# Kernel optimization log

Measured on AMD Instinct MI355X. Metric: run time of the kernel, lower is better.

The kernel has to match this reference:

```python
import jax, jax.numpy as jnp
import numpy as np

H = 16        # heads
DH = 64       # dim_head
DM = 1024     # query_dim = context_dim
INNER = H * DH


def setup_inputs() -> dict:
    key = jax.random.key(0)
    ks = jax.random.split(key, 5)
    s = 0.02
    queries = jax.random.normal(ks[0], (2, 2048, DM), dtype=jnp.float32)
    Wq = jax.random.normal(ks[1], (DM, INNER), dtype=jnp.float32) * s
    Wkv = jax.random.normal(ks[2], (DM, 2 * INNER), dtype=jnp.float32) * s
    Wo = jax.random.normal(ks[3], (INNER, DM), dtype=jnp.float32) * s
    bo = jax.random.normal(ks[4], (DM,), dtype=jnp.float32) * s
    return {"queries": queries, "Wq": Wq, "Wkv": Wkv, "Wo": Wo, "bo": bo}


def reference(queries, Wq, Wkv, Wo, bo):
    b, n, _ = queries.shape
    scale = DH ** -0.5
    q = queries @ Wq                       # [b, n, inner]
    kv = queries @ Wkv                     # self-attention: context = queries
    k, v = jnp.split(kv, 2, axis=-1)
    # b n (h d) -> b h n d
    split_heads = lambda t: t.reshape(b, n, H, DH).transpose(0, 2, 1, 3)
    q, k, v = map(split_heads, (q, k, v))
    sim = jnp.einsum('bhid,bhjd->bhij', q, k) * scale
    attn = jax.nn.softmax(sim, axis=-1)    # dropout is identity (p=0 / eval)
    out = jnp.einsum('bhij,bhjd->bhid', attn, v)
    out = out.transpose(0, 2, 1, 3).reshape(b, n, INNER)
    return out @ Wo + bo
```

## Files before the change

kernel.cpp:

```cpp
#include <hip/hip_runtime.h>
#include <math.h>
#include <stdint.h>

typedef _Float16 half8v __attribute__((ext_vector_type(8)));
typedef _Float16 half4v __attribute__((ext_vector_type(4)));
typedef _Float16 half2v __attribute__((ext_vector_type(2)));
typedef __fp16 fp16x2 __attribute__((ext_vector_type(2)));
typedef float floatx4 __attribute__((ext_vector_type(4)));

#define MFMA16(a, b, c) __builtin_amdgcn_mfma_f32_16x16x32_f16(a, b, c, 0, 0, 0)

#define QSCALE 0.18033688011112f

__device__ __forceinline__ void gld_lds16(const void* g, void* l) {
  __builtin_amdgcn_global_load_lds(
      (const __attribute__((address_space(1))) uint32_t*)(uintptr_t)g,
      (__attribute__((address_space(3))) uint32_t*)(uintptr_t)l, 16, 0, 0);
}

__device__ __forceinline__ half2v pk16(float a, float b) {
  fp16x2 t = __builtin_amdgcn_cvt_pkrtz(a, b);
  return __builtin_bit_cast(half2v, t);
}

__device__ __forceinline__ int swz(int row, int blk) {
  return row * 64 + ((blk ^ (row & 7)) << 3);
}

__device__ __forceinline__ int vswz(int row, int blk) {
  return row * 32 + ((blk ^ ((row >> 1) & 3)) << 3);
}

__device__ __forceinline__ int gswz(int row, int blk) {
  return row * 32 + ((blk ^ ((row >> 1) & 3)) << 3);
}

__global__ __launch_bounds__(256) void prep(
    const float* __restrict__ X, const float* __restrict__ Wq,
    const float* __restrict__ Wkv, const float* __restrict__ Wo,
    _Float16* __restrict__ X16, _Float16* __restrict__ WqkvT,
    _Float16* __restrict__ WoT)
{
  __shared__ alignas(16) _Float16 Tt[64 * 68];
  const int bid = blockIdx.x;
  if (bid < 2048) {
    size_t gid = (size_t)bid * 256 + threadIdx.x;
    const float4* src = (const float4*)(X) + gid * 2;
    float4 a = src[0], b = src[1];
    half8v h;
    h[0]=(_Float16)a.x; h[1]=(_Float16)a.y; h[2]=(_Float16)a.z; h[3]=(_Float16)a.w;
    h[4]=(_Float16)b.x; h[5]=(_Float16)b.y; h[6]=(_Float16)b.z; h[7]=(_Float16)b.w;
    *((half8v*)X16 + gid) = h;
    return;
  }
  int b = bid - 2048;
  const float* src; _Float16* dst; int N, tk, tn;
  if (b < 256)      { src = Wq;  dst = WqkvT;                 N = 1024; tk = b & 15;        tn = b >> 4; }
  else if (b < 768) { src = Wkv; dst = WqkvT + (size_t)1024 * 1024; N = 2048; tk = (b - 256) & 15; tn = (b - 256) >> 4; }
  else              { src = Wo;  dst = WoT;                   N = 1024; tk = (b - 768) & 15; tn = (b - 768) >> 4; }

  const int t = threadIdx.x;
  {
    int kg = t >> 4, ng = t & 15;
    const float* sp = src + (size_t)(tk * 64 + kg * 4) * N + tn * 64 + ng * 4;
    float4 r0 = *(const float4*)(sp);
    float4 r1 = *(const float4*)(sp + N);
    float4 r2 = *(const float4*)(sp + 2 * N);
    float4 r3 = *(const float4*)(sp + 3 * N);
    half4v h;
    h[0]=(_Float16)r0.x; h[1]=(_Float16)r1.x; h[2]=(_Float16)r2.x; h[3]=(_Float16)r3.x;
    *(half4v*)&Tt[(ng * 4 + 0) * 68 + kg * 4] = h;
    h[0]=(_Float16)r0.y; h[1]=(_Float16)r1.y; h[2]=(_Float16)r2.y; h[3]=(_Float16)r3.y;
    *(half4v*)&Tt[(ng * 4 + 1) * 68 + kg * 4] = h;
    h[0]=(_Float16)r0.z; h[1]=(_Float16)r1.z; h[2]=(_Float16)r2.z; h[3]=(_Float16)r3.z;
    *(half4v*)&Tt[(ng * 4 + 2) * 68 + kg * 4] = h;
    h[0]=(_Float16)r0.w; h[1]=(_Float16)r1.w; h[2]=(_Float16)r2.w; h[3]=(_Float16)r3.w;
    *(half4v*)&Tt[(ng * 4 + 3) * 68 + kg * 4] = h;
  }
  __syncthreads();
  #pragma unroll
  for (int i = 0; i < 2; i++) {
    int idx = t + i * 256;
    int nl = idx >> 3, k8 = (idx & 7) * 8;
    half8v v = *(half8v*)&Tt[nl * 68 + k8];
    *(half8v*)(dst + (size_t)(tn * 64 + nl) * 1024 + tk * 64 + k8) = v;
  }
}

__global__ __launch_bounds__(256) void qkv_gemm(
    const _Float16* __restrict__ X16, const _Float16* __restrict__ WqkvT,
    _Float16* __restrict__ q_ws, _Float16* __restrict__ k_ws,
    _Float16* __restrict__ vT_ws)
{
  constexpr int K = 1024;
  __shared__ alignas(16) _Float16 Tt[128 * 136];
  _Float16* As = Tt;
  _Float16* Bs = Tt + 4096;

  const int m0 = blockIdx.x * 128;
  const int n0 = blockIdx.y * 128;

  const int tid  = threadIdx.x;
  const int wave = tid >> 6, lane = tid & 63;
  const int qd = lane >> 4, l15 = lane & 15;
  const int wr = (wave >> 1) * 64, wc = (wave & 1) * 64;
  const int r0i = tid >> 2;
  const int cbs = (((tid & 3) ^ ((r0i >> 1) & 3))) * 8;

  floatx4 acc[4][4] = {};

  for (int k0 = 0; k0 < K; k0 += 32) {
    gld_lds16(X16 + (size_t)(m0 + r0i) * K + k0 + cbs, &As[tid * 8]);
    gld_lds16(X16 + (size_t)(m0 + 64 + r0i) * K + k0 + cbs, &As[(tid + 256) * 8]);
    gld_lds16(WqkvT + (size_t)(n0 + r0i) * K + k0 + cbs, &Bs[tid * 8]);
    gld_lds16(WqkvT + (size_t)(n0 + 64 + r0i) * K + k0 + cbs, &Bs[(tid + 256) * 8]);
    __syncthreads();
    half8v a[4], b[4];
    #pragma unroll
    for (int it = 0; it < 4; it++)
      a[it] = *(half8v*)&As[gswz(wr + it * 16 + l15, qd)];
    #pragma unroll
    for (int jt = 0; jt < 4; jt++)
      b[jt] = *(half8v*)&Bs[gswz(wc + jt * 16 + l15, qd)];
    #pragma unroll
    for (int it = 0; it < 4; it++)
      #pragma unroll
      for (int jt = 0; jt < 4; jt++)
        acc[it][jt] = MFMA16(a[it], b[jt], acc[it][jt]);
    __syncthreads();
  }

  if (n0 < 2048) {
    #pragma unroll
    for (int it = 0; it < 4; it++) {
      #pragma unroll
      for (int jt = 0; jt < 4; jt++) {
        #pragma unroll
        for (int r = 0; r < 4; r++) {
          int m = m0 + wr + it * 16 + qd * 4 + r;
          int n = n0 + wc + jt * 16 + l15;
          float val = acc[it][jt][r];
          int bb = m >> 11, nn = m & 2047;
          if (n0 < 1024) {
            int h = n >> 6, d = n & 63;
            q_ws[(((size_t)bb * 16 + h) * 2048 + nn) * 64 + d] = (_Float16)(val * QSCALE);
          } else {
            int c = n - 1024, h = c >> 6, d = c & 63;
            k_ws[(((size_t)bb * 16 + h) * 2048 + nn) * 64 + d] = (_Float16)val;
          }
        }
      }
    }
  } else {
    #pragma unroll
    for (int it = 0; it < 4; it++) {
      #pragma unroll
      for (int jt = 0; jt < 4; jt++) {
        #pragma unroll
        for (int r = 0; r < 4; r++) {
          int ml = wr + it * 16 + qd * 4 + r;
          int nl = wc + jt * 16 + l15;
          Tt[nl * 136 + ml] = (_Float16)acc[it][jt][r];
        }
      }
    }
    __syncthreads();
    int row = tid >> 1;
    int mh  = (tid & 1) * 64;
    int c   = (n0 - 2048) + row;
    int bb  = m0 >> 11;
    int nnb = (m0 & 2047) + mh;
    _Float16* dstp =
        vT_ws + (((size_t)bb * 16 + (c >> 6)) * 64 + (c & 63)) * 2048 + nnb;
    #pragma unroll
    for (int i = 0; i < 8; i++)
      *(half8v*)(dstp + i * 8) = *(half8v*)&Tt[row * 136 + mh + i * 8];
  }
}

__global__ __launch_bounds__(256, 2) void attn_kernel(
    const _Float16* __restrict__ q_ws, const _Float16* __restrict__ k_ws,
    const _Float16* __restrict__ vT_ws, _Float16* __restrict__ aout)
{
  constexpr int N = 2048;
  __shared__ alignas(16) char smem[66560];
  _Float16* Kbase = (_Float16*)smem;
  _Float16* Vbase = (_Float16*)(smem + 32768);
  _Float16* PQ    = (_Float16*)(smem + 49152);

  const int id = blockIdx.x;
  const int bh = ((id >> 8) << 3) | (id & 7);
  const int qt = (id >> 3) & 31;

  const _Float16* Qp = q_ws + (size_t)bh * N * 64;
  const _Float16* Kp = k_ws + (size_t)bh * N * 64;
  const _Float16* Vp = vT_ws + (size_t)bh * 64 * N;

  const int tid = threadIdx.x, wave = tid >> 6, lane = tid & 63;
  const int qd = lane >> 4, l15 = lane & 15;
  const int q0 = qt * 64;
  const int wkv = wave * 32;

  _Float16* Ps = PQ + wave * 2048;
  _Float16* Vs = Vbase + wave * 2048;

  const int krr = lane >> 3, kcb = (lane & 7) ^ krr;
  const int vrr = lane >> 2, vcb = (lane & 3) ^ ((lane >> 3) & 3);

  auto stage_k = [&](int il, int buf) {
    const _Float16* src = Kp + (size_t)(wkv + il * 128) * 64;
    _Float16* dst = Kbase + (wave * 2 + buf) * 2048;
    #pragma unroll
    for (int j = 0; j < 4; j++)
      gld_lds16(src + (size_t)(j * 8 + krr) * 64 + kcb * 8,
                dst + (j * 64 + lane) * 8);
  };
  auto stage_v = [&](int il) {
    const _Float16* src = Vp + wkv + il * 128;
    #pragma unroll
    for (int j = 0; j < 4; j++)
      gld_lds16(src + (size_t)(j * 16 + (vrr & 15)) * N + vcb * 8,
                Vs + (j * 64 + lane) * 8);
  };

  #pragma unroll
  for (int i = 0; i < 2; i++) {
    int idx = tid + i * 256;
    int r = idx >> 3, cb = (idx ^ r) & 7;
    gld_lds16(Qp + (size_t)(q0 + r) * 64 + cb * 8, PQ + idx * 8);
  }
  stage_k(0, 0);
  stage_v(0);
  stage_k(1, 1);

  asm volatile("s_waitcnt vmcnt(12)" ::: "memory");
  __builtin_amdgcn_s_barrier();
  __builtin_amdgcn_sched_barrier(0);

  half8v qf[4][2];
  #pragma unroll
  for (int m = 0; m < 4; m++)
    #pragma unroll
    for (int ks = 0; ks < 2; ks++)
      qf[m][ks] = *(half8v*)&PQ[swz(m * 16 + l15, ks * 4 + qd)];

  asm volatile("s_waitcnt lgkmcnt(0)" ::: "memory");
  __builtin_amdgcn_s_barrier();
  __builtin_amdgcn_sched_barrier(0);

  const half8v ones = {(_Float16)1, (_Float16)1, (_Float16)1, (_Float16)1,
                       (_Float16)1, (_Float16)1, (_Float16)1, (_Float16)1};
  floatx4 o[4][4] = {};
  floatx4 ol[4] = {};

  #pragma unroll 2
  for (int i = 0; i < 16; ++i) {
    if (i < 15) asm volatile("s_waitcnt vmcnt(8)" ::: "memory");
    else        asm volatile("s_waitcnt vmcnt(4)" ::: "memory");
    __builtin_amdgcn_sched_barrier(0);

    const _Float16* Kb = Kbase + (wave * 2 + (i & 1)) * 2048;

    floatx4 s[2][4] = {};
    #pragma unroll
    for (int ks = 0; ks < 2; ks++) {
      half8v kf0 = *(half8v*)&Kb[swz(l15, ks * 4 + qd)];
      half8v kf1 = *(half8v*)&Kb[swz(16 + l15, ks * 4 + qd)];
      __builtin_amdgcn_s_setprio(1);
      #pragma unroll
      for (int m = 0; m < 4; m++) {
        s[0][m] = MFMA16(kf0, qf[m][ks], s[0][m]);
        s[1][m] = MFMA16(kf1, qf[m][ks], s[1][m]);
      }
      __builtin_amdgcn_s_setprio(0);
    }

    #pragma unroll
    for (int m = 0; m < 4; m++)
      #pragma unroll
      for (int nt = 0; nt < 2; nt++) {
        float p0 = __builtin_amdgcn_exp2f(s[nt][m][0]);
        float p1 = __builtin_amdgcn_exp2f(s[nt][m][1]);
        float p2 = __builtin_amdgcn_exp2f(s[nt][m][2]);
        float p3 = __builtin_amdgcn_exp2f(s[nt][m][3]);
        half2v h01 = pk16(p0, p1);
        half2v h23 = pk16(p2, p3);
        half4v pk;
        pk[0] = h01[0]; pk[1] = h01[1]; pk[2] = h23[0]; pk[3] = h23[1];
        *(half4v*)&Ps[vswz(m * 16 + l15, 2 * nt + (qd >> 1)) + (qd & 1) * 4] = pk;
      }

    if (i < 15) asm volatile("s_waitcnt vmcnt(4)" ::: "memory");
    else        asm volatile("s_waitcnt vmcnt(0)" ::: "memory");
    __builtin_amdgcn_sched_barrier(0);

    half8v pf[4], vfr[4];
    #pragma unroll
    for (int m = 0; m < 4; m++)
      pf[m] = *(half8v*)&Ps[vswz(m * 16 + l15, qd)];
    #pragma unroll
    for (int dt = 0; dt < 4; dt++)
      vfr[dt] = *(half8v*)&Vs[vswz(dt * 16 + l15, qd)];

    asm volatile("s_waitcnt lgkmcnt(0)" ::: "memory");
    __builtin_amdgcn_sched_barrier(0);

    if (i <= 14) stage_v(i + 1);
    if (i <= 13) stage_k(i + 2, i & 1);
    __builtin_amdgcn_sched_barrier(0);

    __builtin_amdgcn_s_setprio(1);
    #pragma unroll
    for (int m = 0; m < 4; m++)
      ol[m] = MFMA16(pf[m], ones, ol[m]);
    #pragma unroll
    for (int m = 0; m < 4; m++)
      #pragma unroll
      for (int dt = 0; dt < 4; dt++)
        o[m][dt] = MFMA16(pf[m], vfr[dt], o[m][dt]);
    __builtin_amdgcn_s_setprio(0);
  }

  __syncthreads();
  float* sc    = (float*)smem;
  float* ls_sc = (float*)(smem + 65536);
  float* myp = sc + wave * 4096;
  #pragma unroll
  for (int m = 0; m < 4; m++)
    #pragma unroll
    for (int r = 0; r < 4; r++) {
      int row = m * 16 + qd * 4 + r;
      myp[row * 64 +  0 + l15] = o[m][0][r];
      myp[row * 64 + 16 + l15] = o[m][1][r];
      myp[row * 64 + 32 + l15] = o[m][2][r];
      myp[row * 64 + 48 + l15] = o[m][3][r];
      ls_sc[wave * 64 + row] = ol[m][r];
    }
  __syncthreads();

  const int bb = bh >> 4, hh = bh & 15;
  #pragma unroll
  for (int j = 0; j < 4; j++) {
    int row = wave * 16 + j * 4 + qd;
    floatx4 a0 = *(floatx4*)&sc[(size_t)(0 * 64 + row) * 64 + l15 * 4];
    floatx4 a1 = *(floatx4*)&sc[(size_t)(1 * 64 + row) * 64 + l15 * 4];
    floatx4 a2 = *(floatx4*)&sc[(size_t)(2 * 64 + row) * 64 + l15 * 4];
    floatx4 a3 = *(floatx4*)&sc[(size_t)(3 * 64 + row) * 64 + l15 * 4];
    floatx4 sum = (a0 + a1) + (a2 + a3);
    float ls = ls_sc[row] + ls_sc[64 + row] + ls_sc[128 + row] + ls_sc[192 + row];
    float inv = 1.0f / ls;
    half2v h01 = pk16(sum[0] * inv, sum[1] * inv);
    half2v h23 = pk16(sum[2] * inv, sum[3] * inv);
    half4v hv;
    hv[0] = h01[0]; hv[1] = h01[1]; hv[2] = h23[0]; hv[3] = h23[1];
    *(half4v*)(aout + ((size_t)(bb * 2048 + q0 + row)) * 1024 + hh * 64 + l15 * 4) = hv;
  }
}

__global__ __launch_bounds__(256) void out_gemm(
    const _Float16* __restrict__ A, const _Float16* __restrict__ WoT,
    const float* __restrict__ bo, float* __restrict__ Out)
{
  constexpr int K = 1024;
  __shared__ alignas(16) _Float16 As[64 * 64];
  __shared__ alignas(16) _Float16 Bs[128 * 64];

  const int m0 = blockIdx.x * 64;
  const int n0 = blockIdx.y * 128;
  const int tid = threadIdx.x;
  const int wave = tid >> 6, lane = tid & 63;
  const int qd = lane >> 4, l15 = lane & 15;
  const int wr = (wave >> 1) * 32, wc = (wave & 1) * 64;

  floatx4 acc[2][4] = {};

  for (int k0 = 0; k0 < K; k0 += 64) {
    #pragma unroll
    for (int i = 0; i < 2; i++) {
      int idx = tid + i * 256;
      int r = idx >> 3, cb = (idx ^ r) & 7;
      gld_lds16(A + (size_t)(m0 + r) * K + k0 + cb * 8, &As[idx * 8]);
    }
    #pragma unroll
    for (int i = 0; i < 4; i++) {
      int idx = tid + i * 256;
      int r = idx >> 3, cb = (idx ^ r) & 7;
      gld_lds16(WoT + (size_t)(n0 + r) * K + k0 + cb * 8, &Bs[idx * 8]);
    }
    __syncthreads();
    half8v a[2][2], b[4][2];
    #pragma unroll
    for (int it = 0; it < 2; it++)
      #pragma unroll
      for (int ks = 0; ks < 2; ks++)
        a[it][ks] = *(half8v*)&As[swz(wr + it * 16 + l15, ks * 4 + qd)];
    #pragma unroll
    for (int jt = 0; jt < 4; jt++)
      #pragma unroll
      for (int ks = 0; ks < 2; ks++)
        b[jt][ks] = *(half8v*)&Bs[swz(wc + jt * 16 + l15, ks * 4 + qd)];
    #pragma unroll
    for (int ks = 0; ks < 2; ks++)
      #pragma unroll
      for (int it = 0; it < 2; it++)
        #pragma unroll
        for (int jt = 0; jt < 4; jt++)
          acc[it][jt] = MFMA16(a[it][ks], b[jt][ks], acc[it][jt]);
    __syncthreads();
  }

  #pragma unroll
  for (int it = 0; it < 2; it++) {
    #pragma unroll
    for (int jt = 0; jt < 4; jt++) {
      int n = n0 + wc + jt * 16 + l15;
      float bias = bo[n];
      #pragma unroll
      for (int r = 0; r < 4; r++) {
        int m = m0 + wr + it * 16 + qd * 4 + r;
        Out[(size_t)m * 1024 + n] = acc[it][jt][r] + bias;
      }
    }
  }
}

extern "C" void kernel_launch(void* const* d_in, const int* in_sizes, int n_in,
                              void* d_out, int out_size, void* d_ws, size_t ws_size,
                              hipStream_t stream) {
  const float* X   = (const float*)d_in[0];
  const float* Wq  = (const float*)d_in[1];
  const float* Wkv = (const float*)d_in[2];
  const float* Wo  = (const float*)d_in[3];
  const float* bo  = (const float*)d_in[4];
  float* out = (float*)d_out;

  const size_t M4 = (size_t)4 * 1024 * 1024;
  _Float16* q_ws   = (_Float16*)d_ws;
  _Float16* k_ws   = q_ws + M4;
  _Float16* vT_ws  = k_ws + M4;
  _Float16* X16    = vT_ws + M4;
  _Float16* WqkvT  = X16 + M4;
  _Float16* WoT    = WqkvT + (size_t)3 * 1024 * 1024;
  _Float16* aout   = X16;

  prep<<<3072, 256, 0, stream>>>(X, Wq, Wkv, Wo, X16, WqkvT, WoT);
  qkv_gemm<<<dim3(32, 24), 256, 0, stream>>>(X16, WqkvT, q_ws, k_ws, vT_ws);
  attn_kernel<<<1024, 256, 0, stream>>>(q_ws, k_ws, vT_ws, aout);
  out_gemm<<<dim3(64, 8), 256, 0, stream>>>(aout, WoT, bo, out);
}
```

Measured before the change: 179.0 us.

## Give each wave private double-buffered LDS tiles and drop block barriers in QKV GEMM

Restructures the QKV GEMM main loop so that each wave loads its own 64-row A and B slices into a private double-buffered LDS region, prefetching two K-steps ahead. Progress is ordered with vmcnt/lgkmcnt waits instead of __syncthreads, and the MFMA block runs at raised priority. This removes block-wide barriers and overlaps global-to-LDS loads with compute. In exchange, LDS use grows to 64KB, which may reduce occupancy, and tiles that were shared across waves are now loaded redundantly.

```diff
diff --git a/kernel.cpp b/kernel.cpp
--- a/kernel.cpp
+++ b/kernel.cpp
@@ -28,10 +28,6 @@
 }
 
 __device__ __forceinline__ int vswz(int row, int blk) {
-  return row * 32 + ((blk ^ ((row >> 1) & 3)) << 3);
-}
-
-__device__ __forceinline__ int gswz(int row, int blk) {
   return row * 32 + ((blk ^ ((row >> 1) & 3)) << 3);
 }
 
@@ -93,9 +89,8 @@
     _Float16* __restrict__ vT_ws)
 {
   constexpr int K = 1024;
-  __shared__ alignas(16) _Float16 Tt[128 * 136];
-  _Float16* As = Tt;
-  _Float16* Bs = Tt + 4096;
+  __shared__ alignas(16) char qsmem[65536];
+  _Float16* Tt = (_Float16*)qsmem;
 
   const int m0 = blockIdx.x * 128;
   const int n0 = blockIdx.y * 128;
@@ -104,30 +99,58 @@
   const int wave = tid >> 6, lane = tid & 63;
   const int qd = lane >> 4, l15 = lane & 15;
   const int wr = (wave >> 1) * 64, wc = (wave & 1) * 64;
-  const int r0i = tid >> 2;
-  const int cbs = (((tid & 3) ^ ((r0i >> 1) & 3))) * 8;
+
+  _Float16* Aw = (_Float16*)(qsmem + wave * 16384);
+  _Float16* Bw = (_Float16*)(qsmem + wave * 16384 + 8192);
+
+  const int vrr = lane >> 2, vcb = (lane & 3) ^ ((lane >> 3) & 3);
+
+  const _Float16* Asrc = X16   + (size_t)(m0 + wr + vrr) * K + vcb * 8;
+  const _Float16* Bsrc = WqkvT + (size_t)(n0 + wc + vrr) * K + vcb * 8;
+
+  auto stage = [&](const _Float16* src, _Float16* dstbase, int t) {
+    #pragma unroll
+    for (int j = 0; j < 4; j++)
+      gld_lds16(src + (size_t)(j * 16) * K + t * 32,
+                dstbase + (j * 64 + lane) * 8);
+  };
+
+  stage(Asrc, Aw, 0);        stage(Bsrc, Bw, 0);
+  stage(Asrc, Aw + 2048, 1); stage(Bsrc, Bw + 2048, 1);
 
   floatx4 acc[4][4] = {};
 
-  for (int k0 = 0; k0 < K; k0 += 32) {
-    gld_lds16(X16 + (size_t)(m0 + r0i) * K + k0 + cbs, &As[tid * 8]);
-    gld_lds16(X16 + (size_t)(m0 + 64 + r0i) * K + k0 + cbs, &As[(tid + 256) * 8]);
-    gld_lds16(WqkvT + (size_t)(n0 + r0i) * K + k0 + cbs, &Bs[tid * 8]);
-    gld_lds16(WqkvT + (size_t)(n0 + 64 + r0i) * K + k0 + cbs, &Bs[(tid + 256) * 8]);
-    __syncthreads();
+  for (int i = 0; i < 32; ++i) {
+    if (i < 31) asm volatile("s_waitcnt vmcnt(8)" ::: "memory");
+    else        asm volatile("s_waitcnt vmcnt(0)" ::: "memory");
+    __builtin_amdgcn_sched_barrier(0);
+
+    const _Float16* Ab = Aw + (i & 1) * 2048;
+    const _Float16* Bb = Bw + (i & 1) * 2048;
     half8v a[4], b[4];
     #pragma unroll
     for (int it = 0; it < 4; it++)
-      a[it] = *(half8v*)&As[gswz(wr + it * 16 + l15, qd)];
+      a[it] = *(half8v*)&Ab[vswz(it * 16 + l15, qd)];
     #pragma unroll
     for (int jt = 0; jt < 4; jt++)
-      b[jt] = *(half8v*)&Bs[gswz(wc + jt * 16 + l15, qd)];
+      b[jt] = *(half8v*)&Bb[vswz(jt * 16 + l15, qd)];
+
+    asm volatile("s_waitcnt lgkmcnt(0)" ::: "memory");
+    __builtin_amdgcn_sched_barrier(0);
+
+    if (i <= 29) {
+      stage(Asrc, Aw + (i & 1) * 2048, i + 2);
+      stage(Bsrc, Bw + (i & 1) * 2048, i + 2);
+    }
+    __builtin_amdgcn_sched_barrier(0);
+
+    __builtin_amdgcn_s_setprio(1);
     #pragma unroll
     for (int it = 0; it < 4; it++)
       #pragma unroll
       for (int jt = 0; jt < 4; jt++)
         acc[it][jt] = MFMA16(a[it], b[jt], acc[it][jt]);
-    __syncthreads();
+    __builtin_amdgcn_s_setprio(0);
   }
 
   if (n0 < 2048) {
@@ -152,6 +175,7 @@
       }
     }
   } else {
+    __syncthreads();
     #pragma unroll
     for (int it = 0; it < 4; it++) {
       #pragma unroll
```

After: 186.6 us. +4.2%, slower.

## Split attention block into 8 waves sharing K/V tiles across query halves

Applied to the files above, without the earlier changes.

The attention block grows from 4 to 8 waves. Each group of 4 waves handles 32 of the 64 query rows, and both groups read the same double-buffered K and V tiles in shared memory, where V was previously held per wave. K and V are now staged two tiles ahead behind a block barrier, and the final cross-wave reduction runs in two passes to fit the smaller scratch area. This is meant to raise the wave count per CU, to halve per-wave register accumulators, and to reuse each K/V tile across more query rows. In exchange it adds a per-iteration block barrier, raises shared memory per block to 80KB, and uses launch bounds (512,4) that may not be achievable.

```diff
diff --git a/kernel.cpp b/kernel.cpp
--- a/kernel.cpp
+++ b/kernel.cpp
@@ -178,15 +178,15 @@
   }
 }
 
-__global__ __launch_bounds__(256, 2) void attn_kernel(
+__global__ __launch_bounds__(512, 4) void attn_kernel(
     const _Float16* __restrict__ q_ws, const _Float16* __restrict__ k_ws,
     const _Float16* __restrict__ vT_ws, _Float16* __restrict__ aout)
 {
   constexpr int N = 2048;
-  __shared__ alignas(16) char smem[66560];
+  __shared__ alignas(16) char smem[81920];
   _Float16* Kbase = (_Float16*)smem;
   _Float16* Vbase = (_Float16*)(smem + 32768);
-  _Float16* PQ    = (_Float16*)(smem + 49152);
+  _Float16* PQ    = (_Float16*)(smem + 65536);
 
   const int id = blockIdx.x;
   const int bh = ((id >> 8) << 3) | (id & 7);
@@ -199,50 +199,46 @@
   const int tid = threadIdx.x, wave = tid >> 6, lane = tid & 63;
   const int qd = lane >> 4, l15 = lane & 15;
   const int q0 = qt * 64;
-  const int wkv = wave * 32;
-
-  _Float16* Ps = PQ + wave * 2048;
-  _Float16* Vs = Vbase + wave * 2048;
+  const int kvw = wave & 3, qw = wave >> 2;
+  const int wkv = kvw * 32;
+
+  _Float16* Ps = PQ + wave * 1024;
 
   const int krr = lane >> 3, kcb = (lane & 7) ^ krr;
   const int vrr = lane >> 2, vcb = (lane & 3) ^ ((lane >> 3) & 3);
 
   auto stage_k = [&](int il, int buf) {
     const _Float16* src = Kp + (size_t)(wkv + il * 128) * 64;
-    _Float16* dst = Kbase + (wave * 2 + buf) * 2048;
+    _Float16* dst = Kbase + (kvw * 2 + buf) * 2048;
     #pragma unroll
     for (int j = 0; j < 4; j++)
       gld_lds16(src + (size_t)(j * 8 + krr) * 64 + kcb * 8,
                 dst + (j * 64 + lane) * 8);
   };
-  auto stage_v = [&](int il) {
+  auto stage_v = [&](int il, int buf) {
     const _Float16* src = Vp + wkv + il * 128;
+    _Float16* dst = Vbase + (kvw * 2 + buf) * 2048;
     #pragma unroll
     for (int j = 0; j < 4; j++)
-      gld_lds16(src + (size_t)(j * 16 + (vrr & 15)) * N + vcb * 8,
-                Vs + (j * 64 + lane) * 8);
+      gld_lds16(src + (size_t)(j * 16 + vrr) * N + vcb * 8,
+                dst + (j * 64 + lane) * 8);
   };
 
-  #pragma unroll
-  for (int i = 0; i < 2; i++) {
-    int idx = tid + i * 256;
-    int r = idx >> 3, cb = (idx ^ r) & 7;
-    gld_lds16(Qp + (size_t)(q0 + r) * 64 + cb * 8, PQ + idx * 8);
-  }
-  stage_k(0, 0);
-  stage_v(0);
-  stage_k(1, 1);
-
-  asm volatile("s_waitcnt vmcnt(12)" ::: "memory");
+  { int r = tid >> 3, cb = (tid ^ r) & 7;
+    gld_lds16(Qp + (size_t)(q0 + r) * 64 + cb * 8, PQ + tid * 8); }
+  stage_k(0, 0); stage_v(0, 0);
+  stage_k(1, 1); stage_v(1, 1);
+
+  asm volatile("s_waitcnt vmcnt(16)" ::: "memory");
   __builtin_amdgcn_s_barrier();
   __builtin_amdgcn_sched_barrier(0);
 
-  half8v qf[4][2];
+  half8v qf[2][2];
   #pragma unroll
-  for (int m = 0; m < 4; m++)
+  for (int m = 0; m < 2; m++)
     #pragma unroll
     for (int ks = 0; ks < 2; ks++)
-      qf[m][ks] = *(half8v*)&PQ[swz(m * 16 + l15, ks * 4 + qd)];
+      qf[m][ks] = *(half8v*)&PQ[swz(qw * 32 + m * 16 + l15, ks * 4 + qd)];
 
   asm volatile("s_waitcnt lgkmcnt(0)" ::: "memory");
   __builtin_amdgcn_s_barrier();
@@ -250,33 +246,50 @@
 
   const half8v ones = {(_Float16)1, (_Float16)1, (_Float16)1, (_Float16)1,
                        (_Float16)1, (_Float16)1, (_Float16)1, (_Float16)1};
-  floatx4 o[4][4] = {};
-  floatx4 ol[4] = {};
-
-  #pragma unroll 2
+  floatx4 o[2][4] = {};
+  floatx4 ol[2] = {};
+
   for (int i = 0; i < 16; ++i) {
     if (i < 15) asm volatile("s_waitcnt vmcnt(8)" ::: "memory");
-    else        asm volatile("s_waitcnt vmcnt(4)" ::: "memory");
+    else        asm volatile("s_waitcnt vmcnt(0)" ::: "memory");
     __builtin_amdgcn_sched_barrier(0);
 
-    const _Float16* Kb = Kbase + (wave * 2 + (i & 1)) * 2048;
-
-    floatx4 s[2][4] = {};
+    const _Float16* Kb = Kbase + (kvw * 2 + (i & 1)) * 2048;
+    const _Float16* Vb = Vbase + (kvw * 2 + (i & 1)) * 2048;
+
+    half8v kf[2][2], vfr[4];
     #pragma unroll
     for (int ks = 0; ks < 2; ks++) {
-      half8v kf0 = *(half8v*)&Kb[swz(l15, ks * 4 + qd)];
-      half8v kf1 = *(half8v*)&Kb[swz(16 + l15, ks * 4 + qd)];
-      __builtin_amdgcn_s_setprio(1);
-      #pragma unroll
-      for (int m = 0; m < 4; m++) {
-        s[0][m] = MFMA16(kf0, qf[m][ks], s[0][m]);
-        s[1][m] = MFMA16(kf1, qf[m][ks], s[1][m]);
-      }
-      __builtin_amdgcn_s_setprio(0);
-    }
-
-    #pragma unroll
-    for (int m = 0; m < 4; m++)
+      kf[ks][0] = *(half8v*)&Kb[swz(l15, ks * 4 + qd)];
+      kf[ks][1] = *(half8v*)&Kb[swz(16 + l15, ks * 4 + qd)];
+    }
+    #pragma unroll
+    for (int dt = 0; dt < 4; dt++)
+      vfr[dt] = *(half8v*)&Vb[vswz(dt * 16 + l15, qd)];
+
+    asm volatile("s_waitcnt lgkmcnt(0)" ::: "memory");
+    __builtin_amdgcn_sched_barrier(0);
+
+    if (i <= 13) {
+      __builtin_amdgcn_s_barrier();
+      stage_k(i + 2, i & 1);
+      stage_v(i + 2, i & 1);
+    }
+    __builtin_amdgcn_sched_barrier(0);
+
+    floatx4 s[2][2] = {};
+    __builtin_amdgcn_s_setprio(1);
+    #pragma unroll
+    for (int ks = 0; ks < 2; ks++)
+      #pragma unroll
+      for (int m = 0; m < 2; m++) {
+        s[0][m] = MFMA16(kf[ks][0], qf[m][ks], s[0][m]);
+        s[1][m] = MFMA16(kf[ks][1], qf[m][ks], s[1][m]);
+      }
+    __builtin_amdgcn_s_setprio(0);
+
+    #pragma unroll
+    for (int m = 0; m < 2; m++)
       #pragma unroll
       for (int nt = 0; nt < 2; nt++) {
         float p0 = __builtin_amdgcn_exp2f(s[nt][m][0]);
@@ -290,31 +303,16 @@
         *(half4v*)&Ps[vswz(m * 16 + l15, 2 * nt + (qd >> 1)) + (qd & 1) * 4] = pk;
       }
 
-    if (i < 15) asm volatile("s_waitcnt vmcnt(4)" ::: "memory");
-    else        asm volatile("s_waitcnt vmcnt(0)" ::: "memory");
-    __builtin_amdgcn_sched_barrier(0);
-
-    half8v pf[4], vfr[4];
-    #pragma unroll
-    for (int m = 0; m < 4; m++)
+    half8v pf[2];
+    #pragma unroll
+    for (int m = 0; m < 2; m++)
       pf[m] = *(half8v*)&Ps[vswz(m * 16 + l15, qd)];
-    #pragma unroll
-    for (int dt = 0; dt < 4; dt++)
-      vfr[dt] = *(half8v*)&Vs[vswz(dt * 16 + l15, qd)];
-
-    asm volatile("s_waitcnt lgkmcnt(0)" ::: "memory");
-    __builtin_amdgcn_sched_barrier(0);
-
-    if (i <= 14) stage_v(i + 1);
-    if (i <= 13) stage_k(i + 2, i & 1);
-    __builtin_amdgcn_sched_barrier(0);
-
     __builtin_amdgcn_s_setprio(1);
     #pragma unroll
-    for (int m = 0; m < 4; m++)
+    for (int m = 0; m < 2; m++)
       ol[m] = MFMA16(pf[m], ones, ol[m]);
     #pragma unroll
-    for (int m = 0; m < 4; m++)
+    for (int m = 0; m < 2; m++)
       #pragma unroll
       for (int dt = 0; dt < 4; dt++)
         o[m][dt] = MFMA16(pf[m], vfr[dt], o[m][dt]);
@@ -322,38 +320,43 @@
   }
 
   __syncthreads();
-  float* sc    = (float*)smem;
-  float* ls_sc = (float*)(smem + 65536);
-  float* myp = sc + wave * 4096;
+  float* sc = (float*)smem;
+  float* ls = (float*)(smem + 36864);
+  const int bb = bh >> 4, hh = bh & 15;
+
   #pragma unroll
-  for (int m = 0; m < 4; m++)
-    #pragma unroll
-    for (int r = 0; r < 4; r++) {
-      int row = m * 16 + qd * 4 + r;
-      myp[row * 64 +  0 + l15] = o[m][0][r];
-      myp[row * 64 + 16 + l15] = o[m][1][r];
-      myp[row * 64 + 32 + l15] = o[m][2][r];
-      myp[row * 64 + 48 + l15] = o[m][3][r];
-      ls_sc[wave * 64 + row] = ol[m][r];
-    }
-  __syncthreads();
-
-  const int bb = bh >> 4, hh = bh & 15;
-  #pragma unroll
-  for (int j = 0; j < 4; j++) {
-    int row = wave * 16 + j * 4 + qd;
-    floatx4 a0 = *(floatx4*)&sc[(size_t)(0 * 64 + row) * 64 + l15 * 4];
-    floatx4 a1 = *(floatx4*)&sc[(size_t)(1 * 64 + row) * 64 + l15 * 4];
-    floatx4 a2 = *(floatx4*)&sc[(size_t)(2 * 64 + row) * 64 + l15 * 4];
-    floatx4 a3 = *(floatx4*)&sc[(size_t)(3 * 64 + row) * 64 + l15 * 4];
-    floatx4 sum = (a0 + a1) + (a2 + a3);
-    float ls = ls_sc[row] + ls_sc[64 + row] + ls_sc[128 + row] + ls_sc[192 + row];
-    float inv = 1.0f / ls;
-    half2v h01 = pk16(sum[0] * inv, sum[1] * inv);
-    half2v h23 = pk16(sum[2] * inv, sum[3] * inv);
-    half4v hv;
-    hv[0] = h01[0]; hv[1] = h01[1]; hv[2] = h23[0]; hv[3] = h23[1];
-    *(half4v*)(aout + ((size_t)(bb * 2048 + q0 + row)) * 1024 + hh * 64 + l15 * 4) = hv;
+  for (int pass = 0; pass < 2; pass++) {
+    if (qw == pass) {
+      float* my = sc + kvw * 2176;
+      #pragma unroll
+      for (int m = 0; m < 2; m++) {
+        #pragma unroll
+        for (int dt = 0; dt < 4; dt++)
+          #pragma unroll
+          for (int r = 0; r < 4; r++)
+            my[(m * 16 + qd * 4 + r) * 68 + dt * 16 + l15] = o[m][dt][r];
+        #pragma unroll
+        for (int r = 0; r < 4; r++)
+          ls[kvw * 32 + m * 16 + qd * 4 + r] = ol[m][r];
+      }
+    }
+    __syncthreads();
+    {
+      int row = tid >> 4, c0 = (tid & 15) * 4;
+      float lsv = ls[row] + ls[32 + row] + ls[64 + row] + ls[96 + row];
+      float inv = 1.0f / lsv;
+      floatx4 acc = {};
+      #pragma unroll
+      for (int w = 0; w < 4; w++)
+        acc += *(const floatx4*)&sc[w * 2176 + row * 68 + c0];
+      half2v h01 = pk16(acc[0] * inv, acc[1] * inv);
+      half2v h23 = pk16(acc[2] * inv, acc[3] * inv);
+      half4v hv;
+      hv[0] = h01[0]; hv[1] = h01[1]; hv[2] = h23[0]; hv[3] = h23[1];
+      *(half4v*)(aout + ((size_t)(bb * 2048 + q0 + pass * 32 + row)) * 1024 +
+                 hh * 64 + c0) = hv;
+    }
+    if (pass == 0) __syncthreads();
   }
 }
 
@@ -445,6 +448,6 @@
 
   prep<<<3072, 256, 0, stream>>>(X, Wq, Wkv, Wo, X16, WqkvT, WoT);
   qkv_gemm<<<dim3(32, 24), 256, 0, stream>>>(X16, WqkvT, q_ws, k_ws, vT_ws);
-  attn_kernel<<<1024, 256, 0, stream>>>(q_ws, k_ws, vT_ws, aout);
+  attn_kernel<<<1024, 512, 0, stream>>>(q_ws, k_ws, vT_ws, aout);
   out_gemm<<<dim3(64, 8), 256, 0, stream>>>(aout, WoT, bo, out);
 }
```

New measurement: 187.1 us. 1.05x slower.

## Software-pipeline QK^T of next tile with softmax/PV of previous, double-buffer V

Applied to the files above, without the earlier changes.

Restructures the attention inner loop so the QK^T MFMAs for tile i run ahead of the exp/PV work for tile i-1, using two ping-pong score register sets. V staging becomes double-buffered in LDS, which raises shared memory to 80 KB, and the K/V async loads are reissued at new points with adjusted vmcnt waits. The goal is to overlap MFMA work with exp and LDS traffic and hide global-load latency. The cost is more registers and LDS, which may reduce occupancy below two blocks per CU.

```diff
diff --git a/kernel.cpp b/kernel.cpp
--- a/kernel.cpp
+++ b/kernel.cpp
@@ -183,10 +183,10 @@
     const _Float16* __restrict__ vT_ws, _Float16* __restrict__ aout)
 {
   constexpr int N = 2048;
-  __shared__ alignas(16) char smem[66560];
+  __shared__ alignas(16) char smem[81920];
   _Float16* Kbase = (_Float16*)smem;
   _Float16* Vbase = (_Float16*)(smem + 32768);
-  _Float16* PQ    = (_Float16*)(smem + 49152);
+  _Float16* PQ    = (_Float16*)(smem + 65536);
 
   const int id = blockIdx.x;
   const int bh = ((id >> 8) << 3) | (id & 7);
@@ -202,7 +202,6 @@
   const int wkv = wave * 32;
 
   _Float16* Ps = PQ + wave * 2048;
-  _Float16* Vs = Vbase + wave * 2048;
 
   const int krr = lane >> 3, kcb = (lane & 7) ^ krr;
   const int vrr = lane >> 2, vcb = (lane & 3) ^ ((lane >> 3) & 3);
@@ -215,12 +214,13 @@
       gld_lds16(src + (size_t)(j * 8 + krr) * 64 + kcb * 8,
                 dst + (j * 64 + lane) * 8);
   };
-  auto stage_v = [&](int il) {
+  auto stage_v = [&](int il, int buf) {
     const _Float16* src = Vp + wkv + il * 128;
+    _Float16* dst = Vbase + (wave * 2 + buf) * 2048;
     #pragma unroll
     for (int j = 0; j < 4; j++)
-      gld_lds16(src + (size_t)(j * 16 + (vrr & 15)) * N + vcb * 8,
-                Vs + (j * 64 + lane) * 8);
+      gld_lds16(src + (size_t)(j * 16 + vrr) * N + vcb * 8,
+                dst + (j * 64 + lane) * 8);
   };
 
   #pragma unroll
@@ -230,8 +230,8 @@
     gld_lds16(Qp + (size_t)(q0 + r) * 64 + cb * 8, PQ + idx * 8);
   }
   stage_k(0, 0);
-  stage_v(0);
   stage_k(1, 1);
+  stage_v(0, 0);
 
   asm volatile("s_waitcnt vmcnt(12)" ::: "memory");
   __builtin_amdgcn_s_barrier();
@@ -252,63 +252,71 @@
                        (_Float16)1, (_Float16)1, (_Float16)1, (_Float16)1};
   floatx4 o[4][4] = {};
   floatx4 ol[4] = {};
-
-  #pragma unroll 2
-  for (int i = 0; i < 16; ++i) {
-    if (i < 15) asm volatile("s_waitcnt vmcnt(8)" ::: "memory");
-    else        asm volatile("s_waitcnt vmcnt(4)" ::: "memory");
-    __builtin_amdgcn_sched_barrier(0);
-
+  floatx4 sA[2][4], sB[2][4];
+
+  auto qk_step = [&](int i, floatx4 (&scur)[2][4]) {
+    if (i >= 1 && i <= 14) asm volatile("s_waitcnt vmcnt(12)" ::: "memory");
+    else                   asm volatile("s_waitcnt vmcnt(8)"  ::: "memory");
+    __builtin_amdgcn_sched_barrier(0);
     const _Float16* Kb = Kbase + (wave * 2 + (i & 1)) * 2048;
-
-    floatx4 s[2][4] = {};
+    half8v kf[2][2];
     #pragma unroll
     for (int ks = 0; ks < 2; ks++) {
-      half8v kf0 = *(half8v*)&Kb[swz(l15, ks * 4 + qd)];
-      half8v kf1 = *(half8v*)&Kb[swz(16 + l15, ks * 4 + qd)];
-      __builtin_amdgcn_s_setprio(1);
+      kf[ks][0] = *(half8v*)&Kb[swz(l15, ks * 4 + qd)];
+      kf[ks][1] = *(half8v*)&Kb[swz(16 + l15, ks * 4 + qd)];
+    }
+    asm volatile("s_waitcnt lgkmcnt(0)" ::: "memory");
+    __builtin_amdgcn_sched_barrier(0);
+    if (i <= 13) stage_k(i + 2, i & 1);
+    __builtin_amdgcn_sched_barrier(0);
+    #pragma unroll
+    for (int nt = 0; nt < 2; nt++)
+      #pragma unroll
+      for (int m = 0; m < 4; m++)
+        scur[nt][m] = floatx4{0.f, 0.f, 0.f, 0.f};
+    __builtin_amdgcn_s_setprio(1);
+    #pragma unroll
+    for (int ks = 0; ks < 2; ks++)
       #pragma unroll
       for (int m = 0; m < 4; m++) {
-        s[0][m] = MFMA16(kf0, qf[m][ks], s[0][m]);
-        s[1][m] = MFMA16(kf1, qf[m][ks], s[1][m]);
+        scur[0][m] = MFMA16(kf[ks][0], qf[m][ks], scur[0][m]);
+        scur[1][m] = MFMA16(kf[ks][1], qf[m][ks], scur[1][m]);
       }
-      __builtin_amdgcn_s_setprio(0);
-    }
-
+    __builtin_amdgcn_s_setprio(0);
+  };
+
+  auto sm_pv_step = [&](int i, floatx4 (&sprev)[2][4]) {
     #pragma unroll
     for (int m = 0; m < 4; m++)
       #pragma unroll
       for (int nt = 0; nt < 2; nt++) {
-        float p0 = __builtin_amdgcn_exp2f(s[nt][m][0]);
-        float p1 = __builtin_amdgcn_exp2f(s[nt][m][1]);
-        float p2 = __builtin_amdgcn_exp2f(s[nt][m][2]);
-        float p3 = __builtin_amdgcn_exp2f(s[nt][m][3]);
+        float p0 = __builtin_amdgcn_exp2f(sprev[nt][m][0]);
+        float p1 = __builtin_amdgcn_exp2f(sprev[nt][m][1]);
+        float p2 = __builtin_amdgcn_exp2f(sprev[nt][m][2]);
+        float p3 = __builtin_amdgcn_exp2f(sprev[nt][m][3]);
         half2v h01 = pk16(p0, p1);
         half2v h23 = pk16(p2, p3);
         half4v pk;
         pk[0] = h01[0]; pk[1] = h01[1]; pk[2] = h23[0]; pk[3] = h23[1];
         *(half4v*)&Ps[vswz(m * 16 + l15, 2 * nt + (qd >> 1)) + (qd & 1) * 4] = pk;
       }
-
-    if (i < 15) asm volatile("s_waitcnt vmcnt(4)" ::: "memory");
-    else        asm volatile("s_waitcnt vmcnt(0)" ::: "memory");
-    __builtin_amdgcn_sched_barrier(0);
-
     half8v pf[4], vfr[4];
     #pragma unroll
     for (int m = 0; m < 4; m++)
       pf[m] = *(half8v*)&Ps[vswz(m * 16 + l15, qd)];
+    if (i <= 13)       asm volatile("s_waitcnt vmcnt(12)" ::: "memory");
+    else if (i == 14)  asm volatile("s_waitcnt vmcnt(8)"  ::: "memory");
+    else if (i == 15)  asm volatile("s_waitcnt vmcnt(4)"  ::: "memory");
+    else               asm volatile("s_waitcnt vmcnt(0)"  ::: "memory");
+    __builtin_amdgcn_sched_barrier(0);
+    const _Float16* Vb = Vbase + (wave * 2 + ((i - 1) & 1)) * 2048;
     #pragma unroll
     for (int dt = 0; dt < 4; dt++)
-      vfr[dt] = *(half8v*)&Vs[vswz(dt * 16 + l15, qd)];
-
+      vfr[dt] = *(half8v*)&Vb[vswz(dt * 16 + l15, qd)];
     asm volatile("s_waitcnt lgkmcnt(0)" ::: "memory");
     __builtin_amdgcn_sched_barrier(0);
-
-    if (i <= 14) stage_v(i + 1);
-    if (i <= 13) stage_k(i + 2, i & 1);
-    __builtin_amdgcn_sched_barrier(0);
-
+    if (i <= 14) stage_v(i + 1, (i + 1) & 1);
+    __builtin_amdgcn_sched_barrier(0);
     __builtin_amdgcn_s_setprio(1);
     #pragma unroll
     for (int m = 0; m < 4; m++)
@@ -319,7 +327,20 @@
       for (int dt = 0; dt < 4; dt++)
         o[m][dt] = MFMA16(pf[m], vfr[dt], o[m][dt]);
     __builtin_amdgcn_s_setprio(0);
-  }
+  };
+
+  qk_step(0, sA);
+  stage_v(1, 1);
+
+  for (int i = 1; i <= 15; i += 2) {
+    qk_step(i, sB);
+    sm_pv_step(i, sA);
+    if (i + 1 <= 15) {
+      qk_step(i + 1, sA);
+      sm_pv_step(i + 1, sB);
+    }
+  }
+  sm_pv_step(16, sB);
 
   __syncthreads();
   float* sc    = (float*)smem;
```

After: 178.5 us. No clear change (-0.3%).
